# Optimization experiments

Hardware: AMD Instinct MI355X
Metric: run time of the kernel (lower is better)

The kernel has to match this reference:

```python
import jax, jax.numpy as jnp
import numpy as np

N_NODES = 20000
N_EDGES = 640000
D = 128


def setup_inputs() -> dict:
    key = jax.random.key(0)
    ks = jax.random.split(key, 8)
    scale = 1.0 / np.sqrt(D)
    x = jax.random.normal(ks[0], (N_NODES, D), dtype=jnp.float32)
    edge_index = jax.random.randint(ks[1], (2, N_EDGES), 0, N_NODES, dtype=jnp.int64)
    W1_rel = jax.random.normal(ks[2], (D, D), dtype=jnp.float32) * scale
    b1_rel = jnp.zeros((D,), dtype=jnp.float32)
    W1_root = jax.random.normal(ks[3], (D, D), dtype=jnp.float32) * scale
    W2_rel = jax.random.normal(ks[4], (D, D), dtype=jnp.float32) * scale
    b2_rel = jnp.zeros((D,), dtype=jnp.float32)
    W2_root = jax.random.normal(ks[5], (D, D), dtype=jnp.float32) * scale
    return {"x": x, "edge_index": edge_index,
            "W1_rel": W1_rel, "b1_rel": b1_rel, "W1_root": W1_root,
            "W2_rel": W2_rel, "b2_rel": b2_rel, "W2_root": W2_root}


def _graph_conv(x, src, dst, W_rel, b_rel, W_root):
    # sum-aggregate neighbor features: gather from src, scatter-add to dst
    agg = jax.ops.segment_sum(x[src], dst, num_segments=N_NODES)  # [N, D]
    # PyG GraphConv: lin_rel(agg) (with bias) + lin_root(x) (no bias)
    return agg @ W_rel + b_rel + x @ W_root


def reference(x, edge_index, W1_rel, b1_rel, W1_root, W2_rel, b2_rel, W2_root):
    src, dst = edge_index[0], edge_index[1]  # messages flow src (j) -> dst (i)
    h = jax.nn.relu(_graph_conv(x, src, dst, W1_rel, b1_rel, W1_root))
    out = _graph_conv(h, src, dst, W2_rel, b2_rel, W2_root)  # final ReLU stripped
    return out
```

## Files before the change

kernel.cpp:

```cpp
#include <hip/hip_runtime.h>

#define N_NODES 20000
#define N_EDGES 640000
#define D 128
#define CAP 128
#define NBINS 157
#define BINCAP 4608

typedef __attribute__((ext_vector_type(8))) short bf16x8;
typedef __attribute__((ext_vector_type(4))) float f32x4;

__device__ __forceinline__ short f2bf(float f) {
    union { float f; unsigned u; } un; un.f = f;
    unsigned r = un.u + 0x7fff + ((un.u >> 16) & 1);
    return (short)(r >> 16);
}
__device__ __forceinline__ float bflo(unsigned u) { return __uint_as_float(u << 16); }
__device__ __forceinline__ float bfhi(unsigned u) { return __uint_as_float(u & 0xffff0000u); }

__global__ __launch_bounds__(256) void prep_kernel(
    const float* __restrict__ x,
    const int* __restrict__ src, const int* __restrict__ dst,
    const float* __restrict__ W1_rel, const float* __restrict__ W1_root,
    const float* __restrict__ W2_rel, const float* __restrict__ W2_root,
    int* __restrict__ binCursor, unsigned* __restrict__ binned,
    short* __restrict__ xb, short* __restrict__ wpk1, short* __restrict__ wpk2)
{
    const int b = blockIdx.x;
    const int tid = threadIdx.x;
    if (b < 256) {
        __shared__ int hist[NBINS];
        __shared__ int sBase[NBINS];
        __shared__ int sOff[NBINS];
        for (int i = tid; i < NBINS; i += 256) { hist[i] = 0; sOff[i] = 0; }
        __syncthreads();
        const int e0 = b * 2500;
        int d[10], s[10];
#pragma unroll
        for (int k = 0; k < 10; k++) {
            int idx = k * 256 + tid;
            if (idx < 2500) {
                d[k] = dst[e0 + idx];
                s[k] = src[e0 + idx];
                atomicAdd(&hist[d[k] >> 7], 1);
            } else {
                d[k] = -1;
            }
        }
        __syncthreads();
        for (int i = tid; i < NBINS; i += 256)
            sBase[i] = atomicAdd(&binCursor[i], hist[i]);
        __syncthreads();
#pragma unroll
        for (int k = 0; k < 10; k++) {
            if (d[k] >= 0) {
                int bin = d[k] >> 7;
                int off = sBase[bin] + atomicAdd(&sOff[bin], 1);
                if (off < BINCAP)
                    binned[bin * BINCAP + off] =
                        ((unsigned)(d[k] & 127) << 16) | (unsigned)s[k];
            }
        }
    } else if (b < 2756) {
        int i = (b - 256) * 256 + tid;
        float4 v = ((const float4*)x)[i];
        ushort4 o;
        o.x = (unsigned short)f2bf(v.x);
        o.y = (unsigned short)f2bf(v.y);
        o.z = (unsigned short)f2bf(v.z);
        o.w = (unsigned short)f2bf(v.w);
        ((ushort4*)xb)[i] = o;
    } else {
        int pb  = b - 2756;
        int job = pb >> 4;
        int idx = (pb & 15) * 256 + tid;
        const float* Wrel  = job ? W2_rel  : W1_rel;
        const float* Wroot = job ? W2_root : W1_root;
        short* Wpk = job ? wpk2 : wpk1;
        int lane = idx & 63;
        int ct   = (idx >> 6) & 7;
        int t    = idx >> 9;
        const float* W = (t < 4) ? Wrel : Wroot;
        int k0  = (t & 3) * 32 + (lane >> 4) * 8;
        int col = ct * 16 + (lane & 15);
        bf16x8 pk;
#pragma unroll
        for (int j = 0; j < 8; j++)
            pk[j] = f2bf(W[(size_t)(k0 + j) * D + col]);
        ((bf16x8*)Wpk)[idx] = pk;
    }
}

__global__ __launch_bounds__(256) void binplace_kernel(
    const unsigned* __restrict__ binned, const int* __restrict__ binCursor,
    unsigned short* __restrict__ buckets, int* __restrict__ cnt)
{
    __shared__ int lcnt[128];
    const int bin = blockIdx.x;
    const int tid = threadIdx.x;
    if (tid < 128) lcnt[tid] = 0;
    __syncthreads();
    int n = binCursor[bin];
    if (n > BINCAP) n = BINCAP;
    const unsigned* rec = binned + bin * BINCAP;
    for (int i = tid; i < n; i += 256) {
        unsigned u = rec[i];
        int nl = (int)(u >> 16);
        int slot = atomicAdd(&lcnt[nl], 1);
        if (slot < CAP)
            buckets[(((bin << 7) | nl) << 7) + slot] = (unsigned short)(u & 0xffffu);
    }
    __syncthreads();
    int node = (bin << 7) + tid;
    if (tid < 128 && node < N_NODES) cnt[node] = lcnt[tid];
}

template <bool RELU, bool OUT_BF16>
__global__ __launch_bounds__(512) void layer_kernel(
    const short* __restrict__ xin,
    const int* __restrict__ cnt,
    const unsigned short* __restrict__ buckets,
    const short* __restrict__ Wpk,
    const float* __restrict__ brel,
    void* __restrict__ outp)
{
    __shared__ short sAgg[16][136];

    const int tid  = threadIdx.x;
    const int row0 = blockIdx.x * 16;

    {
        const int hw   = tid >> 5;
        const int lane = tid & 31;
        const int node = row0 + hw;
        int n = cnt[node];
        n = (n > CAP) ? CAP : n;
        uint2 idxpk = *(const uint2*)(buckets + (node << 7) + lane * 4);

        float4 acc = make_float4(0.f, 0.f, 0.f, 0.f);
        int i = 0;
        for (; i + 8 <= n; i += 8) {
            int baseLane = i >> 2;
            uint2 u[8];
#pragma unroll
            for (int q = 0; q < 8; q++) {
                unsigned word = __shfl((q & 2) ? idxpk.y : idxpk.x,
                                       baseLane + (q >> 2), 32);
                unsigned sidx = (q & 1) ? (word >> 16) : (word & 0xffffu);
                u[q] = *(const uint2*)(xin + (size_t)sidx * D + lane * 4);
            }
#pragma unroll
            for (int q = 0; q < 8; q++) {
                acc.x += bflo(u[q].x); acc.y += bfhi(u[q].x);
                acc.z += bflo(u[q].y); acc.w += bfhi(u[q].y);
            }
        }
        for (; i < n; i++) {
            unsigned word = __shfl((i & 2) ? idxpk.y : idxpk.x, i >> 2, 32);
            unsigned sidx = (i & 1) ? (word >> 16) : (word & 0xffffu);
            uint2 u0 = *(const uint2*)(xin + (size_t)sidx * D + lane * 4);
            acc.x += bflo(u0.x); acc.y += bfhi(u0.x);
            acc.z += bflo(u0.y); acc.w += bfhi(u0.y);
        }
        ushort4 o;
        o.x = (unsigned short)f2bf(acc.x);
        o.y = (unsigned short)f2bf(acc.y);
        o.z = (unsigned short)f2bf(acc.z);
        o.w = (unsigned short)f2bf(acc.w);
        *(ushort4*)&sAgg[hw][lane * 4] = o;
    }
    __syncthreads();

    const int wave = tid >> 6;
    const int lane = tid & 63;
    const int quad = lane >> 4;
    const int l16  = lane & 15;

    f32x4 acc = (f32x4){0.f, 0.f, 0.f, 0.f};
    const short* arow_x = xin + (size_t)(row0 + l16) * D + quad * 8;
    const bf16x8* wb = (const bf16x8*)Wpk + lane;

#pragma unroll
    for (int t = 0; t < 8; t++) {
        bf16x8 a;
        if (t < 4)
            a = *(const bf16x8*)&sAgg[l16][(t & 3) * 32 + quad * 8];
        else
            a = *(const bf16x8*)(arow_x + (t & 3) * 32);
        bf16x8 bfr = wb[(t * 8 + wave) * 64];
        acc = __builtin_amdgcn_mfma_f32_16x16x32_bf16(a, bfr, acc, 0, 0, 0);
    }

    const int col  = wave * 16 + l16;
    const int orow = row0 + quad * 4;
    const float bias = brel[col];
#pragma unroll
    for (int r = 0; r < 4; r++) {
        float v = acc[r] + bias;
        if (RELU) v = fmaxf(v, 0.f);
        if (OUT_BF16)
            ((short*)outp)[(size_t)(orow + r) * D + col] = f2bf(v);
        else
            ((float*)outp)[(size_t)(orow + r) * D + col] = v;
    }
}

extern "C" void kernel_launch(void* const* d_in, const int* in_sizes, int n_in,
                              void* d_out, int out_size, void* d_ws, size_t ws_size,
                              hipStream_t stream) {
    const float* x       = (const float*)d_in[0];
    const int*   ei      = (const int*)  d_in[1];
    const float* W1_rel  = (const float*)d_in[2];
    const float* b1_rel  = (const float*)d_in[3];
    const float* W1_root = (const float*)d_in[4];
    const float* W2_rel  = (const float*)d_in[5];
    const float* b2_rel  = (const float*)d_in[6];
    const float* W2_root = (const float*)d_in[7];
    float* out = (float*)d_out;

    char* p = (char*)d_ws;
    short* xb   = (short*)p;  p += (size_t)N_NODES * D * 2;
    short* hb   = (short*)p;  p += (size_t)N_NODES * D * 2;
    short* wpk1 = (short*)p;  p += 65536;
    short* wpk2 = (short*)p;  p += 65536;
    int*   cnt  = (int*)p;    p += (size_t)N_NODES * 4;
    unsigned short* buckets = (unsigned short*)p;
    p += (size_t)N_NODES * CAP * 2;
    unsigned* binned = (unsigned*)p;
    p += (size_t)NBINS * BINCAP * 4;
    int* binCursor = (int*)p;

    const int* src = ei;
    const int* dst = ei + N_EDGES;

    const int layerblocks = N_NODES / 16;

    hipMemsetAsync(binCursor, 0, (size_t)NBINS * sizeof(int), stream);
    prep_kernel<<<2788, 256, 0, stream>>>(
        x, src, dst, W1_rel, W1_root, W2_rel, W2_root,
        binCursor, binned, xb, wpk1, wpk2);

    binplace_kernel<<<NBINS, 256, 0, stream>>>(binned, binCursor, buckets, cnt);

    layer_kernel<true, true><<<layerblocks, 512, 0, stream>>>(
        xb, cnt, buckets, wpk1, b1_rel, (void*)hb);

    layer_kernel<false, false><<<layerblocks, 512, 0, stream>>>(
        hb, cnt, buckets, wpk2, b2_rel, (void*)out);
}
```

Before: 149.9 us.

## Bin edges per 16-node tile and build buckets in layer kernel shared memory

Edges are now binned into 1250 bins of 16 destination nodes, one per layer block, and the separate binplace kernel is removed. Each layer block reads its bin's records and builds its per-node source lists in shared memory with LDS atomics, instead of reading global cnt and bucket arrays. This saves a kernel launch and a global write-then-read pass over the buckets. In exchange, the bucket build runs twice, once per layer, and the partition phase uses fewer blocks with a larger histogram.

```diff
diff --git a/kernel.cpp b/kernel.cpp
--- a/kernel.cpp
+++ b/kernel.cpp
@@ -4,8 +4,10 @@
 #define N_EDGES 640000
 #define D 128
 #define CAP 128
-#define NBINS 157
-#define BINCAP 4608
+#define NBINS 1250
+#define BINCAP 768
+#define PA_BLOCKS 128
+#define EPB 5000
 
 typedef __attribute__((ext_vector_type(8))) short bf16x8;
 typedef __attribute__((ext_vector_type(4))) float f32x4;
@@ -28,41 +30,30 @@
 {
     const int b = blockIdx.x;
     const int tid = threadIdx.x;
-    if (b < 256) {
+    if (b < PA_BLOCKS) {
         __shared__ int hist[NBINS];
         __shared__ int sBase[NBINS];
         __shared__ int sOff[NBINS];
         for (int i = tid; i < NBINS; i += 256) { hist[i] = 0; sOff[i] = 0; }
         __syncthreads();
-        const int e0 = b * 2500;
-        int d[10], s[10];
-#pragma unroll
-        for (int k = 0; k < 10; k++) {
-            int idx = k * 256 + tid;
-            if (idx < 2500) {
-                d[k] = dst[e0 + idx];
-                s[k] = src[e0 + idx];
-                atomicAdd(&hist[d[k] >> 7], 1);
-            } else {
-                d[k] = -1;
-            }
-        }
+        const int e0 = b * EPB;
+        for (int idx = tid; idx < EPB; idx += 256)
+            atomicAdd(&hist[dst[e0 + idx] >> 4], 1);
         __syncthreads();
         for (int i = tid; i < NBINS; i += 256)
             sBase[i] = atomicAdd(&binCursor[i], hist[i]);
         __syncthreads();
-#pragma unroll
-        for (int k = 0; k < 10; k++) {
-            if (d[k] >= 0) {
-                int bin = d[k] >> 7;
-                int off = sBase[bin] + atomicAdd(&sOff[bin], 1);
-                if (off < BINCAP)
-                    binned[bin * BINCAP + off] =
-                        ((unsigned)(d[k] & 127) << 16) | (unsigned)s[k];
-            }
-        }
-    } else if (b < 2756) {
-        int i = (b - 256) * 256 + tid;
+        for (int idx = tid; idx < EPB; idx += 256) {
+            int d = dst[e0 + idx];
+            int s = src[e0 + idx];
+            int bin = d >> 4;
+            int off = sBase[bin] + atomicAdd(&sOff[bin], 1);
+            if (off < BINCAP)
+                binned[bin * BINCAP + off] =
+                    ((unsigned)(d & 15) << 16) | (unsigned)s;
+        }
+    } else if (b < PA_BLOCKS + 2500) {
+        int i = (b - PA_BLOCKS) * 256 + tid;
         float4 v = ((const float4*)x)[i];
         ushort4 o;
         o.x = (unsigned short)f2bf(v.x);
@@ -71,7 +62,7 @@
         o.w = (unsigned short)f2bf(v.w);
         ((ushort4*)xb)[i] = o;
     } else {
-        int pb  = b - 2756;
+        int pb  = b - (PA_BLOCKS + 2500);
         int job = pb >> 4;
         int idx = (pb & 15) * 256 + tid;
         const float* Wrel  = job ? W2_rel  : W1_rel;
@@ -91,51 +82,44 @@
     }
 }
 
-__global__ __launch_bounds__(256) void binplace_kernel(
-    const unsigned* __restrict__ binned, const int* __restrict__ binCursor,
-    unsigned short* __restrict__ buckets, int* __restrict__ cnt)
-{
-    __shared__ int lcnt[128];
-    const int bin = blockIdx.x;
-    const int tid = threadIdx.x;
-    if (tid < 128) lcnt[tid] = 0;
-    __syncthreads();
-    int n = binCursor[bin];
-    if (n > BINCAP) n = BINCAP;
-    const unsigned* rec = binned + bin * BINCAP;
-    for (int i = tid; i < n; i += 256) {
-        unsigned u = rec[i];
-        int nl = (int)(u >> 16);
-        int slot = atomicAdd(&lcnt[nl], 1);
-        if (slot < CAP)
-            buckets[(((bin << 7) | nl) << 7) + slot] = (unsigned short)(u & 0xffffu);
-    }
-    __syncthreads();
-    int node = (bin << 7) + tid;
-    if (tid < 128 && node < N_NODES) cnt[node] = lcnt[tid];
-}
-
 template <bool RELU, bool OUT_BF16>
 __global__ __launch_bounds__(512) void layer_kernel(
     const short* __restrict__ xin,
-    const int* __restrict__ cnt,
-    const unsigned short* __restrict__ buckets,
+    const unsigned* __restrict__ binned,
+    const int* __restrict__ binCursor,
     const short* __restrict__ Wpk,
     const float* __restrict__ brel,
     void* __restrict__ outp)
 {
+    __shared__ unsigned short sBkt[16][CAP];
+    __shared__ int scnt[16];
     __shared__ short sAgg[16][136];
 
     const int tid  = threadIdx.x;
-    const int row0 = blockIdx.x * 16;
+    const int bin  = blockIdx.x;
+    const int row0 = bin * 16;
+
+    if (tid < 16) scnt[tid] = 0;
+    __syncthreads();
+    {
+        int n = binCursor[bin];
+        if (n > BINCAP) n = BINCAP;
+        const unsigned* rec = binned + bin * BINCAP;
+        for (int i = tid; i < n; i += 512) {
+            unsigned u = rec[i];
+            int nl = (int)(u >> 16);
+            int slot = atomicAdd(&scnt[nl], 1);
+            if (slot < CAP) sBkt[nl][slot] = (unsigned short)(u & 0xffffu);
+        }
+    }
+    __syncthreads();
 
     {
         const int hw   = tid >> 5;
         const int lane = tid & 31;
-        const int node = row0 + hw;
-        int n = cnt[node];
+        int n = scnt[hw];
         n = (n > CAP) ? CAP : n;
-        uint2 idxpk = *(const uint2*)(buckets + (node << 7) + lane * 4);
+        uint2 idxpk = *(const uint2*)&sBkt[hw][lane * 4];
 
         float4 acc = make_float4(0.f, 0.f, 0.f, 0.f);
         int i = 0;
@@ -223,9 +207,6 @@
     short* hb   = (short*)p;  p += (size_t)N_NODES * D * 2;
     short* wpk1 = (short*)p;  p += 65536;
     short* wpk2 = (short*)p;  p += 65536;
-    int*   cnt  = (int*)p;    p += (size_t)N_NODES * 4;
-    unsigned short* buckets = (unsigned short*)p;
-    p += (size_t)N_NODES * CAP * 2;
     unsigned* binned = (unsigned*)p;
     p += (size_t)NBINS * BINCAP * 4;
     int* binCursor = (int*)p;
@@ -233,18 +214,16 @@
     const int* src = ei;
     const int* dst = ei + N_EDGES;
 
-    const int layerblocks = N_NODES / 16;
+    const int layerblocks = NBINS;
 
     hipMemsetAsync(binCursor, 0, (size_t)NBINS * sizeof(int), stream);
-    prep_kernel<<<2788, 256, 0, stream>>>(
+    prep_kernel<<<PA_BLOCKS + 2500 + 32, 256, 0, stream>>>(
         x, src, dst, W1_rel, W1_root, W2_rel, W2_root,
         binCursor, binned, xb, wpk1, wpk2);
 
-    binplace_kernel<<<NBINS, 256, 0, stream>>>(binned, binCursor, buckets, cnt);
-
     layer_kernel<true, true><<<layerblocks, 512, 0, stream>>>(
-        xb, cnt, buckets, wpk1, b1_rel, (void*)hb);
+        xb, binned, binCursor, wpk1, b1_rel, (void*)hb);
 
     layer_kernel<false, false><<<layerblocks, 512, 0, stream>>>(
-        hb, cnt, buckets, wpk2, b2_rel, (void*)out);
-}
+        hb, binned, binCursor, wpk2, b2_rel, (void*)out);
+}
```

Measured after the change: 152.2 us. About the same (+1.5%).
